# Performance work log

Measured on AMD Instinct MI355X. Metric: run time of the kernel, lower is better.

## Reference

```python
import jax, jax.numpy as jnp
import numpy as np

B = 256          # graph pairs
MAX = 64         # max_node_set_size
D = 128          # node_state_dim
E_DIM = 64       # edge embedding dim
NODE_F = 32
EDGE_F = 16
AVG_DEG = 8
PROP_STEPS = 3
TEMP = 0.1


def _sizes():
    qs = 32 + (np.arange(B) % 33)   # query graph sizes in [32,64]
    cs = 33 + (np.arange(B) % 32)   # corpus graph sizes in [33,64]
    return qs, cs


def setup_inputs() -> dict:
    key = jax.random.key(0)
    ks = jax.random.split(key, 12)
    qs, cs = _sizes()
    sizes = np.empty(2 * B, dtype=np.int64)
    sizes[0::2] = qs
    sizes[1::2] = cs
    offsets = np.concatenate([[0], np.cumsum(sizes)])
    N = int(offsets[-1])
    rng = np.random.RandomState(0)
    frm, to, pos = [], [], []
    for g in range(2 * B):
        o, s = int(offsets[g]), int(sizes[g])
        ne = AVG_DEG * s
        frm.append(rng.randint(0, s, ne) + o)
        to.append(rng.randint(0, s, ne) + o)
        b, isq = g // 2, (g % 2 == 0)
        base = (0 if isq else B * MAX) + b * MAX
        pos.append(base + np.arange(s))
    from_idx = jnp.asarray(np.concatenate(frm), dtype=jnp.int32)
    to_idx = jnp.asarray(np.concatenate(to), dtype=jnp.int32)
    node_to_pos = jnp.asarray(np.concatenate(pos), dtype=jnp.int32)
    Etot = int(from_idx.shape[0])

    def w(k, shape):
        return jax.random.normal(k, shape, jnp.float32) * (1.0 / np.sqrt(shape[0]))

    return {
        "node_features": jax.random.normal(ks[0], (N, NODE_F), jnp.float32),
        "edge_features": jax.random.normal(ks[1], (Etot, EDGE_F), jnp.float32),
        "from_idx": from_idx,
        "to_idx": to_idx,
        "node_to_pos": node_to_pos,
        "query_sizes": jnp.asarray(qs, jnp.int32),
        "corpus_sizes": jnp.asarray(cs, jnp.int32),
        "W_node": w(ks[2], (NODE_F, D)), "b_node": jnp.zeros((D,), jnp.float32),
        "W_edge": w(ks[3], (EDGE_F, E_DIM)), "b_edge": jnp.zeros((E_DIM,), jnp.float32),
        "W_msg1": w(ks[4], (2 * D + E_DIM, 2 * D)), "b_msg1": jnp.zeros((2 * D,), jnp.float32),
        "W_msg2": w(ks[5], (2 * D, 2 * D)), "b_msg2": jnp.zeros((2 * D,), jnp.float32),
        "W_upd": w(ks[6], (3 * D, D)), "b_upd": jnp.zeros((D,), jnp.float32),
        "Wa1": w(ks[7], (D, D)), "ba1": jnp.zeros((D,), jnp.float32),
        "Wa2": w(ks[8], (D, D)), "ba2": jnp.zeros((D,), jnp.float32),
    }


def reference(node_features, edge_features, from_idx, to_idx, node_to_pos,
              query_sizes, corpus_sizes, W_node, b_node, W_edge, b_edge,
              W_msg1, b_msg1, W_msg2, b_msg2, W_upd, b_upd, Wa1, ba1, Wa2, ba2):
    N = node_features.shape[0]
    # GraphEncoder: single-layer node / edge MLPs
    h = node_features @ W_node + b_node
    e = edge_features @ W_edge + b_edge
    # GraphPropLayer applied propagation_steps times (residual node update)
    for _ in range(PROP_STEPS):
        edge_in = jnp.concatenate([h[from_idx], h[to_idx], e], axis=-1)  # [E, 2D+E_DIM]
        msg = jax.nn.relu(edge_in @ W_msg1 + b_msg1) @ W_msg2 + b_msg2   # [E, 2D]
        agg = jax.ops.segment_sum(msg, to_idx, num_segments=N)           # [N, 2D]
        h = h + (jnp.concatenate([h, agg], axis=-1) @ W_upd + b_upd)
    # split_and_stack: scatter flat node states into padded [B, MAX, D] query/corpus stacks
    flat = jnp.zeros((2 * B * MAX, D), h.dtype).at[node_to_pos].set(h)
    stacked = flat.reshape(2, B, MAX, D)
    sq, sc = stacked[0], stacked[1]

    def att_feat(x):
        return jax.nn.relu(x @ Wa1 + ba1) @ Wa2 + ba2

    mq = (jnp.arange(MAX)[None, :] < query_sizes[:, None]).astype(h.dtype)   # [B,MAX]
    mc = (jnp.arange(MAX)[None, :] < corpus_sizes[:, None]).astype(h.dtype)
    tq = att_feat(sq) * mq[:, :, None]   # graph_size_to_mask_map masking
    tc = att_feat(sc) * mc[:, :, None]
    logits = jnp.einsum('bqd,bcd->bqc', tq, tc) / TEMP
    pair_mask = mq[:, :, None] * mc[:, None, :]
    logits = jnp.where(pair_mask > 0, logits, -1e9)
    q_to_c = jax.nn.softmax(logits, axis=-1) * mq[:, :, None]   # row-stochastic over corpus
    c_to_q = jax.nn.softmax(logits, axis=-2) * mc[:, None, :]   # column-stochastic over query
    # feature_alignment_score / reversed_feature_alignment_score (hinge alignment)
    q_score = -jax.nn.relu(sq - jnp.einsum('bqc,bcd->bqd', q_to_c, sc)).sum((1, 2))
    c_score = -jax.nn.relu(sc - jnp.einsum('bqc,bqd->bcd', c_to_q, sq)).sum((1, 2))
    return jnp.minimum(q_score, c_score)   # attention_mode = 'min'
```

## Files before the change

### kernel.cpp

```cpp
#include <hip/hip_runtime.h>

#define D 128
#define EDIM 64
#define NODE_F 32
#define EDGE_F 16
#define B_PAIRS 256
#define MAXN 64
#define PROP_STEPS 3

typedef __attribute__((ext_vector_type(4))) short short4v;
typedef __attribute__((ext_vector_type(8))) short short8;
typedef __attribute__((ext_vector_type(16))) float floatx16;

__device__ __forceinline__ short f2bf(float x) {
  unsigned u = __float_as_uint(x);
  u = (u + 0x7fff + ((u >> 16) & 1)) >> 16;
  return (short)u;
}

__device__ __forceinline__ float bf2f(short s) {
  return __uint_as_float(((unsigned)(unsigned short)s) << 16);
}

__global__ __launch_bounds__(256) void init_kernel(
    const float* __restrict__ W_node, const float* __restrict__ W_edge,
    const float* __restrict__ W1, const float* __restrict__ W2,
    const float* __restrict__ Wu,
    const float* __restrict__ Wa1, const float* __restrict__ Wa2,
    short* __restrict__ Wfn, short* __restrict__ Wfe,
    short* __restrict__ Wf1a, short* __restrict__ Wf1b, short* __restrict__ Wf1e,
    short* __restrict__ Wf2, short* __restrict__ Wfu,
    short* __restrict__ Wfa1, short* __restrict__ Wfa2,
    const int* __restrict__ to_idx, int* __restrict__ deg,
    int* __restrict__ inv, int E)
{
  int bid = blockIdx.x;
  int t = threadIdx.x;
  if (bid >= 916) {
    int b2 = bid - 916;
    for (int e = b2 * 256 + t; e < E; e += 256 * 256)
      atomicAdd(&deg[to_idx[e]], 1);
    for (int i = b2 * 256 + t; i < 2 * B_PAIRS * MAXN; i += 256 * 256)
      inv[i] = -1;
    return;
  }
  int idx = bid * 256 + t;
  if (idx < 4096) {
    int step = idx >> 11, hi = (idx >> 10) & 1;
    int n = (idx >> 3) & 127, j = idx & 7;
    int k = step * 16 + hi * 8 + j;
    Wfn[idx] = f2bf(W_node[(size_t)k * 128 + n]);
  } else if (idx < 5120) {
    int i = idx - 4096;
    int hi = (i >> 9) & 1, n = (i >> 3) & 63, j = i & 7;
    int k = hi * 8 + j;
    Wfe[i] = f2bf(W_edge[(size_t)k * 64 + n]);
  } else if (idx < 37888) {
    int i = idx - 5120;
    int step = i >> 12, hi = (i >> 11) & 1;
    int n = (i >> 3) & 255, j = i & 7;
    int k = step * 16 + hi * 8 + j;
    Wf1a[i] = f2bf(W1[(size_t)k * 256 + n]);
  } else if (idx < 70656) {
    int i = idx - 37888;
    int step = i >> 12, hi = (i >> 11) & 1;
    int n = (i >> 3) & 255, j = i & 7;
    int k = step * 16 + hi * 8 + j;
    Wf1b[i] = f2bf(W1[(size_t)(128 + k) * 256 + n]);
  } else if (idx < 87040) {
    int i = idx - 70656;
    int step = i >> 12, hi = (i >> 11) & 1;
    int n = (i >> 3) & 255, j = i & 7;
    int k = step * 16 + hi * 8 + j;
    Wf1e[i] = f2bf(W1[(size_t)(256 + k) * 256 + n]);
  } else if (idx < 152576) {
    int i = idx - 87040;
    int step = i >> 12, hi = (i >> 11) & 1;
    int n = (i >> 3) & 255, j = i & 7;
    int k = step * 16 + hi * 8 + j;
    Wf2[i] = f2bf(W2[(size_t)k * 256 + n]);
  } else if (idx < 201728) {
    int i = idx - 152576;
    int step = i >> 11, hi = (i >> 10) & 1;
    int n = (i >> 3) & 127, j = i & 7;
    int k = step * 16 + hi * 8 + j;
    Wfu[i] = f2bf(Wu[(size_t)k * 128 + n]);
  } else if (idx < 218112) {
    int i = idx - 201728;
    int step = i >> 11, hi = (i >> 10) & 1;
    int n = (i >> 3) & 127, j = i & 7;
    int k = step * 16 + hi * 8 + j;
    Wfa1[i] = f2bf(Wa1[(size_t)k * 128 + n]);
  } else if (idx < 234496) {
    int i = idx - 218112;
    int step = i >> 11, hi = (i >> 10) & 1;
    int n = (i >> 3) & 127, j = i & 7;
    int k = step * 16 + hi * 8 + j;
    Wfa2[i] = f2bf(Wa2[(size_t)k * 128 + n]);
  }
}

__global__ __launch_bounds__(1024) void scan1(const int* __restrict__ deg,
                                              int* __restrict__ partials, int N)
{
  __shared__ int red[16];
  int t = threadIdx.x;
  int n = blockIdx.x * 1024 + t;
  int v = (n < N) ? deg[n] : 0;
  for (int off = 32; off > 0; off >>= 1) v += __shfl_down(v, off);
  if ((t & 63) == 0) red[t >> 6] = v;
  __syncthreads();
  if (t == 0) {
    int s = 0;
    #pragma unroll
    for (int i = 0; i < 16; i++) s += red[i];
    partials[blockIdx.x] = s;
  }
}

__global__ __launch_bounds__(64) void scan2(int* __restrict__ partials,
                                            int* __restrict__ offsets, int B, int N)
{
  __shared__ int sp[64];
  int t = threadIdx.x;
  sp[t] = (t < B) ? partials[t] : 0;
  __syncthreads();
  if (t == 0) {
    int run = 0;
    for (int i = 0; i < B; i++) { int v = sp[i]; sp[i] = run; run += v; }
    offsets[N] = run;
  }
  __syncthreads();
  if (t < B) partials[t] = sp[t];
}

__global__ __launch_bounds__(1024) void scan3(const int* __restrict__ deg,
                                              const int* __restrict__ partials,
                                              int* __restrict__ offsets,
                                              int* __restrict__ cursor,
                                              int* __restrict__ zflag,
                                              const int* __restrict__ pos,
                                              int* __restrict__ inv, int N)
{
  __shared__ int s[1024];
  int t = threadIdx.x;
  int n = blockIdx.x * 1024 + t;
  int d = (n < N) ? deg[n] : 0;
  s[t] = d;
  __syncthreads();
  for (int off = 1; off < 1024; off <<= 1) {
    int v = 0;
    if (t >= off) v = s[t - off];
    __syncthreads();
    if (t >= off) s[t] += v;
    __syncthreads();
  }
  if (n < N) {
    int off = partials[blockIdx.x] + s[t] - d;
    offsets[n] = off; cursor[n] = off;
    zflag[n] = (d == 0) || ((off >> 6) != ((off + d - 1) >> 6)) ? 1 : 0;
    inv[pos[n]] = n;
  }
}

__global__ __launch_bounds__(256) void scatter_csr(const int* __restrict__ to_idx,
                                                   int* __restrict__ cursor,
                                                   int* __restrict__ elist, int E)
{
  for (int e = blockIdx.x * 256 + threadIdx.x; e < E; e += gridDim.x * 256) {
    int pos = atomicAdd(&cursor[to_idx[e]], 1);
    elist[pos] = e;
  }
}

__global__ __launch_bounds__(256, 3) void enc_nodes_p(
    const float* __restrict__ nf, const short* __restrict__ Wfn,
    const float* __restrict__ b_node, float* __restrict__ h,
    short* __restrict__ hb,
    const short* __restrict__ Wf1a, const short* __restrict__ Wf1b,
    short* __restrict__ P1f, short* __restrict__ P2f, int N)
{
  __shared__ short sN[32 * 40];
  __shared__ short sH[32 * 136];
  int t = threadIdx.x;
  int ln = t & 63, w = t >> 6;
  int l31 = ln & 31, hi = ln >> 5;
  int n0 = blockIdx.x * 32;

  {
    int r = t >> 3, q = t & 7;
    float4 v = {0.f, 0.f, 0.f, 0.f};
    if (n0 + r < N) v = *(const float4*)(nf + (size_t)(n0 + r) * 32 + q * 4);
    short4v s;
    s[0] = f2bf(v.x); s[1] = f2bf(v.y); s[2] = f2bf(v.z); s[3] = f2bf(v.w);
    *(short4v*)(sN + r * 40 + q * 4) = s;
  }
  __syncthreads();

  int col = w * 32 + l31;
  {
    floatx16 acc;
    #pragma unroll
    for (int i = 0; i < 16; i++) acc[i] = 0.f;
    #pragma unroll
    for (int step = 0; step < 2; step++) {
      short8 a = *(const short8*)(sN + l31 * 40 + step * 16 + hi * 8);
      short8 b = *(const short8*)(Wfn + (size_t)(step * 2 + hi) * 1024 + col * 8);
      acc = __builtin_amdgcn_mfma_f32_32x32x16_bf16(a, b, acc, 0, 0, 0);
    }
    float bv = b_node[col];
    #pragma unroll
    for (int reg = 0; reg < 16; reg++) {
      int row = (reg & 3) + 8 * (reg >> 2) + 4 * hi;
      int n = n0 + row;
      float v = acc[reg] + bv;
      short bf = f2bf(v);
      if (n < N) {
        h[(size_t)n * 128 + col] = v;
        hb[(size_t)n * 128 + col] = bf;
      }
      sH[row * 136 + col] = bf;
    }
  }
  __syncthreads();

  int cb = w * 64;
  const int arow = l31 * 136;
  const int bc0 = (cb + l31) * 8, bc1 = (cb + 32 + l31) * 8;
  floatx16 acc[2][2];
  #pragma unroll
  for (int o = 0; o < 2; o++)
    #pragma unroll
    for (int ct = 0; ct < 2; ct++)
      #pragma unroll
      for (int i = 0; i < 16; i++) acc[o][ct][i] = 0.f;

  #pragma unroll
  for (int step = 0; step < 8; step++) {
    short8 a = *(const short8*)(sH + arow + step * 16 + hi * 8);
    short8 ba0 = *(const short8*)(Wf1a + (size_t)(step * 2 + hi) * 2048 + bc0);
    short8 ba1 = *(const short8*)(Wf1a + (size_t)(step * 2 + hi) * 2048 + bc1);
    short8 bb0 = *(const short8*)(Wf1b + (size_t)(step * 2 + hi) * 2048 + bc0);
    short8 bb1 = *(const short8*)(Wf1b + (size_t)(step * 2 + hi) * 2048 + bc1);
    acc[0][0] = __builtin_amdgcn_mfma_f32_32x32x16_bf16(a, ba0, acc[0][0], 0, 0, 0);
    acc[0][1] = __builtin_amdgcn_mfma_f32_32x32x16_bf16(a, ba1, acc[0][1], 0, 0, 0);
    acc[1][0] = __builtin_amdgcn_mfma_f32_32x32x16_bf16(a, bb0, acc[1][0], 0, 0, 0);
    acc[1][1] = __builtin_amdgcn_mfma_f32_32x32x16_bf16(a, bb1, acc[1][1], 0, 0, 0);
  }

  #pragma unroll
  for (int ct = 0; ct < 2; ct++) {
    int pcol = cb + ct * 32 + l31;
    #pragma unroll
    for (int reg = 0; reg < 16; reg++) {
      int row = (reg & 3) + 8 * (reg >> 2) + 4 * hi;
      int n = n0 + row;
      if (n < N) {
        P1f[(size_t)n * 256 + pcol] = f2bf(acc[0][ct][reg]);
        P2f[(size_t)n * 256 + pcol] = f2bf(acc[1][ct][reg]);
      }
    }
  }
}

__global__ __launch_bounds__(256, 4) void pe_fused(
    const float* __restrict__ ef, const int* __restrict__ elist,
    const short* __restrict__ Wfe, const float* __restrict__ b_edge,
    const short* __restrict__ Wf1e, const float* __restrict__ b1,
    short* __restrict__ Pe, int E)
{
  __shared__ short sE[64 * 24];
  __shared__ short sF[64 * 72];
  __shared__ int eid_s[64];

  int t = threadIdx.x;
  int ln = t & 63, w = t >> 6;
  int l31 = ln & 31, hi = ln >> 5;
  int e0 = blockIdx.x * 64;

  if (t < 64) eid_s[t] = (e0 + t < E) ? elist[e0 + t] : 0;
  __syncthreads();

  {
    int r = t >> 2, q = t & 3;
    float4 v = *(const float4*)(ef + (size_t)eid_s[r] * 16 + q * 4);
    short4v s;
    s[0] = f2bf(v.x); s[1] = f2bf(v.y); s[2] = f2bf(v.z); s[3] = f2bf(v.w);
    *(short4v*)(sE + r * 24 + q * 4) = s;
  }
  __syncthreads();

  {
    int rowb = (w & 1) * 32, cbq = (w >> 1) * 32;
    floatx16 acc;
    #pragma unroll
    for (int i = 0; i < 16; i++) acc[i] = 0.f;
    short8 a = *(const short8*)(sE + (rowb + l31) * 24 + hi * 8);
    short8 b = *(const short8*)(Wfe + (size_t)hi * 512 + (cbq + l31) * 8);
    acc = __builtin_amdgcn_mfma_f32_32x32x16_bf16(a, b, acc, 0, 0, 0);
    int col = cbq + l31;
    float bv = b_edge[col];
    #pragma unroll
    for (int reg = 0; reg < 16; reg++) {
      int row = rowb + (reg & 3) + 8 * (reg >> 2) + 4 * hi;
      sF[row * 72 + col] = f2bf(acc[reg] + bv);
    }
  }
  __syncthreads();

  const int cb = w * 64;
  const int bc0 = (cb + l31) * 8, bc1 = (cb + 32 + l31) * 8;
  floatx16 acc[2][2];
  #pragma unroll
  for (int rg = 0; rg < 2; rg++)
    #pragma unroll
    for (int ct = 0; ct < 2; ct++)
      #pragma unroll
      for (int i = 0; i < 16; i++) acc[rg][ct][i] = 0.f;

  #pragma unroll
  for (int step = 0; step < 4; step++) {
    short8 a0 = *(const short8*)(sF + l31 * 72 + step * 16 + hi * 8);
    short8 a1 = *(const short8*)(sF + (32 + l31) * 72 + step * 16 + hi * 8);
    short8 b0 = *(const short8*)(Wf1e + (size_t)(step * 2 + hi) * 2048 + bc0);
    short8 b1v = *(const short8*)(Wf1e + (size_t)(step * 2 + hi) * 2048 + bc1);
    acc[0][0] = __builtin_amdgcn_mfma_f32_32x32x16_bf16(a0, b0,  acc[0][0], 0, 0, 0);
    acc[0][1] = __builtin_amdgcn_mfma_f32_32x32x16_bf16(a0, b1v, acc[0][1], 0, 0, 0);
    acc[1][0] = __builtin_amdgcn_mfma_f32_32x32x16_bf16(a1, b0,  acc[1][0], 0, 0, 0);
    acc[1][1] = __builtin_amdgcn_mfma_f32_32x32x16_bf16(a1, b1v, acc[1][1], 0, 0, 0);
  }

  #pragma unroll
  for (int rg = 0; rg < 2; rg++)
    #pragma unroll
    for (int ct = 0; ct < 2; ct++) {
      int col = cb + ct * 32 + l31;
      float bv = b1[col];
      #pragma unroll
      for (int reg = 0; reg < 16; reg++) {
        int row = rg * 32 + (reg & 3) + 8 * (reg >> 2) + 4 * hi;
        Pe[(size_t)(e0 + row) * 256 + col] = f2bf(acc[rg][ct][reg] + bv);
      }
    }
}

__global__ __launch_bounds__(256, 4) void msg_agg(
    const short* __restrict__ P1f, const short* __restrict__ P2f,
    const short* __restrict__ Pe,
    const int* __restrict__ from_idx, const int* __restrict__ to_idx,
    const int* __restrict__ elist, const int* __restrict__ offsets,
    float* __restrict__ agg, int E)
{
  __shared__ short sA[64 * 264];
  __shared__ int from_s[64], to_s[64];
  __shared__ int rend_s[64], inter_s[64];

  int t = threadIdx.x;
  int e0 = blockIdx.x * 64;

  if (t < 64) {
    int idx = e0 + t;
    int eid = (idx < E) ? elist[idx] : 0;
    from_s[t] = from_idx[eid];
    to_s[t] = (idx < E) ? to_idx[eid] : -1;
  }
  __syncthreads();

  if (t < 64) {
    int nd = to_s[t];
    bool head = (t == 0) || (nd != to_s[t - 1]);
    if (head && nd >= 0) {
      int re = t + 1;
      while (re < 64 && to_s[re] == nd) re++;
      rend_s[t] = re;
      inter_s[t] = (offsets[nd] == e0 + t) && (offsets[nd + 1] == e0 + re) ? 1 : 0;
    }
  }

  for (int i = t; i < 2048; i += 256) {
    int r = i >> 5, c8 = (i & 31) * 8;
    int nd = to_s[r]; if (nd < 0) nd = 0;
    short8 a = *(const short8*)(P1f + (size_t)from_s[r] * 256 + c8);
    short8 b = *(const short8*)(P2f + (size_t)nd * 256 + c8);
    short8 c = *(const short8*)(Pe + (size_t)(e0 + r) * 256 + c8);
    short8 o;
    #pragma unroll
    for (int j = 0; j < 8; j++)
      o[j] = f2bf(fmaxf(bf2f(a[j]) + bf2f(b[j]) + bf2f(c[j]), 0.f));
    *(short8*)(sA + r * 264 + c8) = o;
  }
  __syncthreads();

  {
    int c = t;
    for (int r = 0; r < 64; ) {
      int nd = to_s[r];
      if (nd < 0) break;
      int re = rend_s[r];
      float a = 0.f;
      for (int i = r; i < re; i++)
        a += bf2f(sA[i * 264 + c]);
      float* dst = agg + (size_t)nd * 256 + c;
      if (inter_s[r]) *dst = a;
      else unsafeAtomicAdd(dst, a);
      r = re;
    }
  }
}

__global__ __launch_bounds__(256, 3) void update_mfma_p(
    float* __restrict__ h, short* __restrict__ hbf, float* __restrict__ agg,
    const short* __restrict__ Wf2, const float* __restrict__ b2,
    const int* __restrict__ deg,
    const short* __restrict__ Wfu, const float* __restrict__ bu,
    const short* __restrict__ Wf1a, const short* __restrict__ Wf1b,
    short* __restrict__ P1f, short* __restrict__ P2f,
    const int* __restrict__ zflag, int want_p, int N)
{
  __shared__ short sA[32 * 392];
  __shared__ short sS[32 * 264];
  __shared__ int zf_s[32];
  __shared__ int deg_s[32];

  int t = threadIdx.x;
  int ln = t & 63, w = t >> 6;
  int l31 = ln & 31, hi = ln >> 5;
  int n0 = blockIdx.x * 32;

  if (t < 32) {
    zf_s[t] = (n0 + t < N) ? zflag[n0 + t] : 0;
    deg_s[t] = (n0 + t < N) ? deg[n0 + t] : 0;
  }

  for (int i = t; i < 512; i += 256) {
    int r = i >> 4, c = i & 15;
    short8 v = {0, 0, 0, 0, 0, 0, 0, 0};
    if (n0 + r < N) v = *(const short8*)(hbf + (size_t)(n0 + r) * 128 + c * 8);
    *(short8*)(sA + r * 392 + c * 8) = v;
  }
  for (int i = t; i < 2048; i += 256) {
    int r = i >> 6, c4 = i & 63;
    int2 pk = {0, 0};
    if (n0 + r < N) {
      float4 v = *(const float4*)(agg + (size_t)(n0 + r) * 256 + c4 * 4);
      pk.x = (int)(unsigned short)f2bf(v.x) | ((int)(unsigned short)f2bf(v.y) << 16);
      pk.y = (int)(unsigned short)f2bf(v.z) | ((int)(unsigned short)f2bf(v.w) << 16);
    }
    *(int2*)(sS + r * 264 + c4 * 4) = pk;
  }
  __syncthreads();

  {
    float4 z = {0.f, 0.f, 0.f, 0.f};
    for (int i = t; i < 2048; i += 256) {
      int r = i >> 6, c4 = i & 63;
      if (n0 + r < N && zf_s[r])
        *(float4*)(agg + (size_t)(n0 + r) * 256 + c4 * 4) = z;
    }
  }

  {
    int cb2 = w * 64;
    const int bc0 = (cb2 + l31) * 8, bc1 = (cb2 + 32 + l31) * 8;
    floatx16 macc[2];
    #pragma unroll
    for (int ct = 0; ct < 2; ct++)
      #pragma unroll
      for (int i = 0; i < 16; i++) macc[ct][i] = 0.f;

    #pragma unroll
    for (int step = 0; step < 16; step++) {
      short8 a = *(const short8*)(sS + l31 * 264 + step * 16 + hi * 8);
      short8 b0 = *(const short8*)(Wf2 + (size_t)(step * 2 + hi) * 2048 + bc0);
      short8 b1v = *(const short8*)(Wf2 + (size_t)(step * 2 + hi) * 2048 + bc1);
      macc[0] = __builtin_amdgcn_mfma_f32_32x32x16_bf16(a, b0,  macc[0], 0, 0, 0);
      macc[1] = __builtin_amdgcn_mfma_f32_32x32x16_bf16(a, b1v, macc[1], 0, 0, 0);
    }

    #pragma unroll
    for (int ct = 0; ct < 2; ct++) {
      int col = cb2 + ct * 32 + l31;
      float bv2 = b2[col];
      #pragma unroll
      for (int reg = 0; reg < 16; reg++) {
        int row = (reg & 3) + 8 * (reg >> 2) + 4 * hi;
        sA[row * 392 + 128 + col] = f2bf(macc[ct][reg] + (float)deg_s[row] * bv2);
      }
    }
  }
  __syncthreads();

  const int arow = l31 * 392;
  const int bcol = (w * 32 + l31) * 8;

  floatx16 acc;
  #pragma unroll
  for (int i = 0; i < 16; i++) acc[i] = 0.f;

  {
    short8 bbuf[3];
    #pragma unroll
    for (int s = 0; s < 3; s++)
      bbuf[s] = *(const short8*)(Wfu + (size_t)(s * 2 + hi) * 1024 + bcol);
    short8 abuf[2];
    abuf[0] = *(const short8*)(sA + arow + hi * 8);
    #pragma unroll
    for (int step = 0; step < 24; step++) {
      if (step + 1 < 24)
        abuf[(step + 1) & 1] = *(const short8*)(sA + arow + (step + 1) * 16 + hi * 8);
      acc = __builtin_amdgcn_mfma_f32_32x32x16_bf16(abuf[step & 1], bbuf[step % 3], acc, 0, 0, 0);
      if (step + 3 < 24)
        bbuf[step % 3] = *(const short8*)(Wfu + (size_t)((step + 3) * 2 + hi) * 1024 + bcol);
    }
  }

  __syncthreads();

  int col = w * 32 + l31;
  float bv = bu[col];
  #pragma unroll
  for (int reg = 0; reg < 16; reg++) {
    int row = (reg & 3) + 8 * (reg >> 2) + 4 * hi;
    int n = n0 + row;
    float nv = 0.f;
    if (n < N) nv = h[(size_t)n * 128 + col] + acc[reg] + bv;
    short bf = f2bf(nv);
    if (n < N) {
      h[(size_t)n * 128 + col] = nv;
      hbf[(size_t)n * 128 + col] = bf;
    }
    sA[row * 392 + col] = bf;
  }

  if (!want_p) return;
  __syncthreads();

  int cb = w * 64;
  const int bc0 = (cb + l31) * 8, bc1 = (cb + 32 + l31) * 8;
  floatx16 pacc[2][2];
  #pragma unroll
  for (int o = 0; o < 2; o++)
    #pragma unroll
    for (int ct = 0; ct < 2; ct++)
      #pragma unroll
      for (int i = 0; i < 16; i++) pacc[o][ct][i] = 0.f;

  #pragma unroll
  for (int step = 0; step < 8; step++) {
    short8 a = *(const short8*)(sA + arow + step * 16 + hi * 8);
    short8 ba0 = *(const short8*)(Wf1a + (size_t)(step * 2 + hi) * 2048 + bc0);
    short8 ba1 = *(const short8*)(Wf1a + (size_t)(step * 2 + hi) * 2048 + bc1);
    short8 bb0 = *(const short8*)(Wf1b + (size_t)(step * 2 + hi) * 2048 + bc0);
    short8 bb1 = *(const short8*)(Wf1b + (size_t)(step * 2 + hi) * 2048 + bc1);
    pacc[0][0] = __builtin_amdgcn_mfma_f32_32x32x16_bf16(a, ba0, pacc[0][0], 0, 0, 0);
    pacc[0][1] = __builtin_amdgcn_mfma_f32_32x32x16_bf16(a, ba1, pacc[0][1], 0, 0, 0);
    pacc[1][0] = __builtin_amdgcn_mfma_f32_32x32x16_bf16(a, bb0, pacc[1][0], 0, 0, 0);
    pacc[1][1] = __builtin_amdgcn_mfma_f32_32x32x16_bf16(a, bb1, pacc[1][1], 0, 0, 0);
  }

  #pragma unroll
  for (int ct = 0; ct < 2; ct++) {
    int pcol = cb + ct * 32 + l31;
    #pragma unroll
    for (int reg = 0; reg < 16; reg++) {
      int row = (reg & 3) + 8 * (reg >> 2) + 4 * hi;
      int n = n0 + row;
      if (n < N) {
        P1f[(size_t)n * 256 + pcol] = f2bf(pacc[0][ct][reg]);
        P2f[(size_t)n * 256 + pcol] = f2bf(pacc[1][ct][reg]);
      }
    }
  }
}

__global__ __launch_bounds__(256, 3) void stack_attfeat(
    const float* __restrict__ h, const int* __restrict__ inv,
    const short* __restrict__ Wfa1, const float* __restrict__ ba1,
    const short* __restrict__ Wfa2, const float* __restrict__ ba2,
    const int* __restrict__ qsizes, const int* __restrict__ csizes,
    float* __restrict__ flat, short* __restrict__ flatT, short* __restrict__ tfb)
{
  __shared__ short sA[64 * 136];
  __shared__ int nd_s[64];

  int t = threadIdx.x;
  int ln = t & 63, w = t >> 6;
  int l31 = ln & 31, hi = ln >> 5;
  int r0 = blockIdx.x * 64;

  if (t < 64) nd_s[t] = inv[r0 + t];
  __syncthreads();

  for (int i = t; i < 1024; i += 256) {
    int r = i >> 4, c = (i & 15) * 8;
    int nd = nd_s[r];
    float4 v0 = {0.f, 0.f, 0.f, 0.f}, v1 = {0.f, 0.f, 0.f, 0.f};
    if (nd >= 0) {
      v0 = *(const float4*)(h + (size_t)nd * 128 + c);
      v1 = *(const float4*)(h + (size_t)nd * 128 + c + 4);
    }
    *(float4*)(flat + (size_t)(r0 + r) * 128 + c) = v0;
    *(float4*)(flat + (size_t)(r0 + r) * 128 + c + 4) = v1;
    short8 s;
    s[0] = f2bf(v0.x); s[1] = f2bf(v0.y); s[2] = f2bf(v0.z); s[3] = f2bf(v0.w);
    s[4] = f2bf(v1.x); s[5] = f2bf(v1.y); s[6] = f2bf(v1.z); s[7] = f2bf(v1.w);
    *(short8*)(sA + r * 136 + c) = s;
  }
  __syncthreads();

  for (int i = t; i < 8192; i += 256) {
    int d = i >> 6, r = i & 63;
    flatT[(size_t)blockIdx.x * 8192 + d * 64 + r] = sA[r * 136 + d];
  }

  const int arow0 = l31 * 136, arow1 = (32 + l31) * 136;
  const int bcol = (w * 32 + l31) * 8;
  int col = w * 32 + l31;

  floatx16 acc[2];
  #pragma unroll
  for (int rg = 0; rg < 2; rg++)
    #pragma unroll
    for (int i = 0; i < 16; i++) acc[rg][i] = 0.f;

  #pragma unroll
  for (int step = 0; step < 8; step++) {
    short8 a0 = *(const short8*)(sA + arow0 + step * 16 + hi * 8);
    short8 a1 = *(const short8*)(sA + arow1 + step * 16 + hi * 8);
    short8 bfr = *(const short8*)(Wfa1 + (size_t)(step * 2 + hi) * 1024 + bcol);
    acc[0] = __builtin_amdgcn_mfma_f32_32x32x16_bf16(a0, bfr, acc[0], 0, 0, 0);
    acc[1] = __builtin_amdgcn_mfma_f32_32x32x16_bf16(a1, bfr, acc[1], 0, 0, 0);
  }

  __syncthreads();
  {
    float bv = ba1[col];
    #pragma unroll
    for (int rg = 0; rg < 2; rg++)
      #pragma unroll
      for (int reg = 0; reg < 16; reg++) {
        int row = rg * 32 + (reg & 3) + 8 * (reg >> 2) + 4 * hi;
        sA[row * 136 + col] = f2bf(fmaxf(acc[rg][reg] + bv, 0.f));
      }
  }
  __syncthreads();

  floatx16 acc2[2];
  #pragma unroll
  for (int rg = 0; rg < 2; rg++)
    #pragma unroll
    for (int i = 0; i < 16; i++) acc2[rg][i] = 0.f;

  #pragma unroll
  for (int step = 0; step < 8; step++) {
    short8 a0 = *(const short8*)(sA + arow0 + step * 16 + hi * 8);
    short8 a1 = *(const short8*)(sA + arow1 + step * 16 + hi * 8);
    short8 bfr = *(const short8*)(Wfa2 + (size_t)(step * 2 + hi) * 1024 + bcol);
    acc2[0] = __builtin_amdgcn_mfma_f32_32x32x16_bf16(a0, bfr, acc2[0], 0, 0, 0);
    acc2[1] = __builtin_amdgcn_mfma_f32_32x32x16_bf16(a1, bfr, acc2[1], 0, 0, 0);
  }

  {
    float bv = ba2[col];
    #pragma unroll
    for (int rg = 0; rg < 2; rg++)
      #pragma unroll
      for (int reg = 0; reg < 16; reg++) {
        int row = r0 + rg * 32 + (reg & 3) + 8 * (reg >> 2) + 4 * hi;
        int part = row >> 14, b = (row >> 6) & 255, pp = row & 63;
        int sz = part ? csizes[b] : qsizes[b];
        float m = (pp < sz) ? 1.f : 0.f;
        tfb[(size_t)row * 128 + col] = f2bf((acc2[rg][reg] + bv) * m);
      }
  }
}

__global__ __launch_bounds__(256, 3) void score_kernel(
    const short* __restrict__ tfb, const float* __restrict__ flat,
    const short* __restrict__ flatT,
    const int* __restrict__ qsizes, const int* __restrict__ csizes,
    float* __restrict__ out)
{
  __shared__ float SL[64 * 65];
  __shared__ float SP2[64 * 65];
  __shared__ float red[8];

  int b = blockIdx.x, t = threadIdx.x;
  int ln = t & 63, w = t >> 6;
  int l31 = ln & 31, hi = ln >> 5;
  const short* tqb = tfb + (size_t)b * 8192;
  const short* tcb = tfb + (size_t)(256 + b) * 8192;
  const float* sq = flat + (size_t)b * 8192;
  const float* sc = flat + (size_t)(256 + b) * 8192;
  const short* sqT = flatT + (size_t)b * 8192;
  const short* scT = flatT + (size_t)(256 + b) * 8192;
  int qs = qsizes[b], cs = csizes[b];

  {
    int rowb = (w & 1) * 32, cbq = (w >> 1) * 32;
    floatx16 acc;
    #pragma unroll
    for (int i = 0; i < 16; i++) acc[i] = 0.f;
    #pragma unroll
    for (int step = 0; step < 8; step++) {
      short8 a  = *(const short8*)(tqb + (size_t)(rowb + l31) * 128 + step * 16 + hi * 8);
      short8 bf = *(const short8*)(tcb + (size_t)(cbq + l31) * 128 + step * 16 + hi * 8);
      acc = __builtin_amdgcn_mfma_f32_32x32x16_bf16(a, bf, acc, 0, 0, 0);
    }
    int ccol = cbq + l31;
    #pragma unroll
    for (int reg = 0; reg < 16; reg++) {
      int qrow = rowb + (reg & 3) + 8 * (reg >> 2) + 4 * hi;
      SL[qrow * 65 + ccol] = (qrow < qs && ccol < cs) ? acc[reg] * 10.0f : -1e9f;
    }
  }
  __syncthreads();

  float rmax = -1e30f, rsum = 0.f;
  if (t < 64) {
    int q = t;
    if (q < qs) {
      for (int c = 0; c < 64; c++) rmax = fmaxf(rmax, SL[q * 65 + c]);
      for (int c = 0; c < 64; c++) rsum += __expf(SL[q * 65 + c] - rmax);
    }
  } else if (t < 128) {
    int c = t - 64;
    if (c < cs) {
      float m = -1e30f;
      for (int q = 0; q < 64; q++) m = fmaxf(m, SL[q * 65 + c]);
      float s = 0.f;
      for (int q = 0; q < 64; q++) s += __expf(SL[q * 65 + c] - m);
      float inv = 1.0f / s;
      for (int q = 0; q < 64; q++) SP2[q * 65 + c] = __expf(SL[q * 65 + c] - m) * inv;
    } else {
      for (int q = 0; q < 64; q++) SP2[q * 65 + c] = 0.f;
    }
  }
  __syncthreads();

  if (t < 64) {
    int q = t;
    if (q < qs) {
      float inv = 1.0f / rsum;
      for (int c = 0; c < 64; c++) SL[q * 65 + c] = __expf(SL[q * 65 + c] - rmax) * inv;
    } else {
      for (int c = 0; c < 64; c++) SL[q * 65 + c] = 0.f;
    }
  }
  __syncthreads();

  int dcol = w * 32 + l31;
  floatx16 accq[2], accc[2];
  #pragma unroll
  for (int rt = 0; rt < 2; rt++) {
    #pragma unroll
    for (int i = 0; i < 16; i++) { accq[rt][i] = 0.f; accc[rt][i] = 0.f; }
  }

  #pragma unroll
  for (int rt = 0; rt < 2; rt++) {
    #pragma unroll
    for (int step = 0; step < 4; step++) {
      int kb = step * 16 + hi * 8;
      int row = rt * 32 + l31;
      short8 a;
      #pragma unroll
      for (int j = 0; j < 8; j++) a[j] = f2bf(SL[row * 65 + kb + j]);
      short8 bf = *(const short8*)(scT + (size_t)dcol * 64 + kb);
      accq[rt] = __builtin_amdgcn_mfma_f32_32x32x16_bf16(a, bf, accq[rt], 0, 0, 0);
    }
  }
  #pragma unroll
  for (int rt = 0; rt < 2; rt++) {
    #pragma unroll
    for (int step = 0; step < 4; step++) {
      int kb = step * 16 + hi * 8;
      int crow = rt * 32 + l31;
      short8 a;
      #pragma unroll
      for (int j = 0; j < 8; j++) a[j] = f2bf(SP2[(kb + j) * 65 + crow]);
      short8 bf = *(const short8*)(sqT + (size_t)dcol * 64 + kb);
      accc[rt] = __builtin_amdgcn_mfma_f32_32x32x16_bf16(a, bf, accc[rt], 0, 0, 0);
    }
  }

  float qpart = 0.f, cpart = 0.f;
  #pragma unroll
  for (int rt = 0; rt < 2; rt++) {
    #pragma unroll
    for (int reg = 0; reg < 16; reg++) {
      int row = rt * 32 + (reg & 3) + 8 * (reg >> 2) + 4 * hi;
      qpart += fmaxf(sq[(size_t)row * 128 + dcol] - accq[rt][reg], 0.f);
      cpart += fmaxf(sc[(size_t)row * 128 + dcol] - accc[rt][reg], 0.f);
    }
  }

  for (int off = 32; off > 0; off >>= 1) {
    qpart += __shfl_down(qpart, off);
    cpart += __shfl_down(cpart, off);
  }
  if ((t & 63) == 0) { red[w] = qpart; red[w + 4] = cpart; }
  __syncthreads();
  if (t == 0) {
    float qsum = red[0] + red[1] + red[2] + red[3];
    float csum = red[4] + red[5] + red[6] + red[7];
    out[b] = fminf(-qsum, -csum);
  }
}

extern "C" void kernel_launch(void* const* d_in, const int* in_sizes, int n_in,
                              void* d_out, int out_size, void* d_ws, size_t ws_size,
                              hipStream_t stream)
{
  const float* nf  = (const float*)d_in[0];
  const float* ef  = (const float*)d_in[1];
  const int* from_idx = (const int*)d_in[2];
  const int* to_idx   = (const int*)d_in[3];
  const int* pos      = (const int*)d_in[4];
  const int* qsz      = (const int*)d_in[5];
  const int* csz      = (const int*)d_in[6];
  const float* W_node = (const float*)d_in[7];
  const float* b_node = (const float*)d_in[8];
  const float* W_edge = (const float*)d_in[9];
  const float* b_edge = (const float*)d_in[10];
  const float* W1 = (const float*)d_in[11];
  const float* b1 = (const float*)d_in[12];
  const float* W2 = (const float*)d_in[13];
  const float* b2 = (const float*)d_in[14];
  const float* Wu = (const float*)d_in[15];
  const float* bu = (const float*)d_in[16];
  const float* Wa1 = (const float*)d_in[17];
  const float* ba1 = (const float*)d_in[18];
  const float* Wa2 = (const float*)d_in[19];
  const float* ba2 = (const float*)d_in[20];
  float* out = (float*)d_out;

  int N = in_sizes[0] / NODE_F;
  int E = in_sizes[1] / EDGE_F;
  int Epad = (E + 63) & ~63;
  int PAD = 2 * B_PAIRS * MAXN;
  int NB = (N + 1023) / 1024;

  float* h    = (float*)d_ws;
  float* agg  = h + (size_t)N * D;
  short* hb   = (short*)(agg + (size_t)N * 256);
  short* P1f  = hb + (size_t)N * D;
  short* P2f  = P1f + (size_t)N * 256;
  short* Wfn  = P2f + (size_t)N * 256;
  short* Wfe  = Wfn + 4096;
  short* Wf1a = Wfe + 1024;
  short* Wf1b = Wf1a + 32768;
  short* Wf1e = Wf1b + 32768;
  short* Wf2  = Wf1e + 16384;
  short* Wfu  = Wf2 + 65536;
  short* Wfa1 = Wfu + 49152;
  short* Wfa2 = Wfa1 + 16384;
  int*   deg     = (int*)(Wfa2 + 16384);
  int*   offsets = deg + N;
  int*   cursor  = offsets + N + 1;
  int*   elist   = cursor + N;
  int*   inv     = elist + E;
  int*   zflag   = inv + PAD;
  int*   partials = zflag + N;
  uintptr_t pb = ((uintptr_t)(partials + 64) + 15) & ~(uintptr_t)15;
  short* Pe = (short*)pb;
  float* flat  = (float*)Pe;
  short* flatT = (short*)(flat + (size_t)PAD * D);
  short* tfb16 = flatT + (size_t)PAD * D;

  hipMemsetAsync(deg, 0, (size_t)N * sizeof(int), stream);
  init_kernel<<<916 + 256, 256, 0, stream>>>(
      W_node, W_edge, W1, W2, Wu, Wa1, Wa2,
      Wfn, Wfe, Wf1a, Wf1b, Wf1e, Wf2, Wfu, Wfa1, Wfa2,
      to_idx, deg, inv, E);
  scan1<<<NB, 1024, 0, stream>>>(deg, partials, N);
  scan2<<<1, 64, 0, stream>>>(partials, offsets, NB, N);
  scan3<<<NB, 1024, 0, stream>>>(deg, partials, offsets, cursor, zflag, pos, inv, N);
  scatter_csr<<<256, 256, 0, stream>>>(to_idx, cursor, elist, E);

  enc_nodes_p<<<(N + 31) / 32, 256, 0, stream>>>(nf, Wfn, b_node, h, hb,
                                                 Wf1a, Wf1b, P1f, P2f, N);
  pe_fused<<<Epad / 64, 256, 0, stream>>>(ef, elist, Wfe, b_edge, Wf1e, b1, Pe, E);

  hipMemsetAsync(agg, 0, (size_t)N * 256 * sizeof(float), stream);

  for (int s = 0; s < PROP_STEPS; s++) {
    msg_agg<<<Epad / 64, 256, 0, stream>>>(P1f, P2f, Pe, from_idx, to_idx, elist, offsets,
                                           agg, E);
    update_mfma_p<<<(N + 31) / 32, 256, 0, stream>>>(h, hb, agg, Wf2, b2, deg,
                                                     Wfu, bu, Wf1a, Wf1b, P1f, P2f, zflag,
                                                     (s + 1 < PROP_STEPS) ? 1 : 0, N);
  }

  stack_attfeat<<<PAD / 64, 256, 0, stream>>>(h, inv, Wfa1, ba1, Wfa2, ba2,
                                              qsz, csz, flat, flatT, tfb16);
  score_kernel<<<B_PAIRS, 256, 0, stream>>>(tfb16, flat, flatT, qsz, csz, out);
}
```

Measured before the change: 456.0 us.

## Fuse message aggregation into node update kernel with shared-memory CSR accumulation

Merges the per-edge message aggregation kernel into the node update kernel. Each block of 32 nodes walks its own CSR edge range and accumulates messages in shared memory instead of doing global atomics into an fp32 agg buffer. This removes the agg round-trip, the zero-flag logic, the memset and one launch per step. P1 is now double-buffered, reusing the agg region, because other blocks still read the previous P1 while this block writes the new one. In exchange the grid is node-based, so blocks with many edges serialize in 32-edge chunks and shared memory per block grows, which may cut occupancy.

```diff
diff --git a/kernel.cpp b/kernel.cpp
--- a/kernel.cpp
+++ b/kernel.cpp
@@ -138,7 +138,6 @@
                                               const int* __restrict__ partials,
                                               int* __restrict__ offsets,
                                               int* __restrict__ cursor,
-                                              int* __restrict__ zflag,
                                               const int* __restrict__ pos,
                                               int* __restrict__ inv, int N)
 {
@@ -158,7 +157,6 @@
   if (n < N) {
     int off = partials[blockIdx.x] + s[t] - d;
     offsets[n] = off; cursor[n] = off;
-    zflag[n] = (d == 0) || ((off >> 6) != ((off + d - 1) >> 6)) ? 1 : 0;
     inv[pos[n]] = n;
   }
 }
@@ -344,119 +342,93 @@
     }
 }
 
-__global__ __launch_bounds__(256, 4) void msg_agg(
-    const short* __restrict__ P1f, const short* __restrict__ P2f,
-    const short* __restrict__ Pe,
+__global__ __launch_bounds__(256, 3) void msg_upd(
+    float* __restrict__ h, short* __restrict__ hbf,
+    const short* __restrict__ P1in, short* __restrict__ P1out,
+    short* __restrict__ P2f, const short* __restrict__ Pe,
     const int* __restrict__ from_idx, const int* __restrict__ to_idx,
     const int* __restrict__ elist, const int* __restrict__ offsets,
-    float* __restrict__ agg, int E)
-{
-  __shared__ short sA[64 * 264];
-  __shared__ int from_s[64], to_s[64];
-  __shared__ int rend_s[64], inter_s[64];
-
-  int t = threadIdx.x;
-  int e0 = blockIdx.x * 64;
-
-  if (t < 64) {
-    int idx = e0 + t;
-    int eid = (idx < E) ? elist[idx] : 0;
-    from_s[t] = from_idx[eid];
-    to_s[t] = (idx < E) ? to_idx[eid] : -1;
-  }
-  __syncthreads();
-
-  if (t < 64) {
-    int nd = to_s[t];
-    bool head = (t == 0) || (nd != to_s[t - 1]);
-    if (head && nd >= 0) {
-      int re = t + 1;
-      while (re < 64 && to_s[re] == nd) re++;
-      rend_s[t] = re;
-      inter_s[t] = (offsets[nd] == e0 + t) && (offsets[nd + 1] == e0 + re) ? 1 : 0;
-    }
-  }
-
-  for (int i = t; i < 2048; i += 256) {
-    int r = i >> 5, c8 = (i & 31) * 8;
-    int nd = to_s[r]; if (nd < 0) nd = 0;
-    short8 a = *(const short8*)(P1f + (size_t)from_s[r] * 256 + c8);
-    short8 b = *(const short8*)(P2f + (size_t)nd * 256 + c8);
-    short8 c = *(const short8*)(Pe + (size_t)(e0 + r) * 256 + c8);
-    short8 o;
-    #pragma unroll
-    for (int j = 0; j < 8; j++)
-      o[j] = f2bf(fmaxf(bf2f(a[j]) + bf2f(b[j]) + bf2f(c[j]), 0.f));
-    *(short8*)(sA + r * 264 + c8) = o;
-  }
-  __syncthreads();
-
-  {
-    int c = t;
-    for (int r = 0; r < 64; ) {
-      int nd = to_s[r];
-      if (nd < 0) break;
-      int re = rend_s[r];
-      float a = 0.f;
-      for (int i = r; i < re; i++)
-        a += bf2f(sA[i * 264 + c]);
-      float* dst = agg + (size_t)nd * 256 + c;
-      if (inter_s[r]) *dst = a;
-      else unsafeAtomicAdd(dst, a);
-      r = re;
-    }
-  }
-}
-
-__global__ __launch_bounds__(256, 3) void update_mfma_p(
-    float* __restrict__ h, short* __restrict__ hbf, float* __restrict__ agg,
+    const int* __restrict__ deg,
     const short* __restrict__ Wf2, const float* __restrict__ b2,
-    const int* __restrict__ deg,
     const short* __restrict__ Wfu, const float* __restrict__ bu,
     const short* __restrict__ Wf1a, const short* __restrict__ Wf1b,
-    short* __restrict__ P1f, short* __restrict__ P2f,
-    const int* __restrict__ zflag, int want_p, int N)
-{
-  __shared__ short sA[32 * 392];
-  __shared__ short sS[32 * 264];
-  __shared__ int zf_s[32];
-  __shared__ int deg_s[32];
+    int want_p, int N)
+{
+  __shared__ float aggL[32 * 256];
+  __shared__ short sStage[32 * 264];
+  __shared__ int to_s[32], from_s[32], deg_s[32];
 
   int t = threadIdx.x;
   int ln = t & 63, w = t >> 6;
   int l31 = ln & 31, hi = ln >> 5;
   int n0 = blockIdx.x * 32;
-
-  if (t < 32) {
-    zf_s[t] = (n0 + t < N) ? zflag[n0 + t] : 0;
-    deg_s[t] = (n0 + t < N) ? deg[n0 + t] : 0;
-  }
+  int nend = (n0 + 32 < N) ? n0 + 32 : N;
+
+  if (t < 32) deg_s[t] = (n0 + t < N) ? deg[n0 + t] : 0;
+  for (int i = t; i < 8192; i += 256) aggL[i] = 0.f;
+  int e_begin = offsets[n0];
+  int e_end = offsets[nend];
+  __syncthreads();
+
+  for (int e0 = e_begin; e0 < e_end; e0 += 32) {
+    if (t < 32) {
+      int idx = e0 + t;
+      if (idx < e_end) {
+        int eid = elist[idx];
+        from_s[t] = from_idx[eid];
+        to_s[t] = to_idx[eid] - n0;
+      } else {
+        to_s[t] = -1;
+      }
+    }
+    __syncthreads();
+
+    for (int i = t; i < 1024; i += 256) {
+      int r = i >> 5, c8 = (i & 31) * 8;
+      int nd = to_s[r];
+      if (nd >= 0) {
+        short8 a = *(const short8*)(P1in + (size_t)from_s[r] * 256 + c8);
+        short8 b = *(const short8*)(P2f + (size_t)(n0 + nd) * 256 + c8);
+        short8 c = *(const short8*)(Pe + (size_t)(e0 + r) * 256 + c8);
+        short8 o;
+        #pragma unroll
+        for (int j = 0; j < 8; j++)
+          o[j] = f2bf(fmaxf(bf2f(a[j]) + bf2f(b[j]) + bf2f(c[j]), 0.f));
+        *(short8*)(sStage + r * 264 + c8) = o;
+      }
+    }
+    __syncthreads();
+
+    {
+      int c = t;
+      for (int r = 0; r < 32; ) {
+        int nd = to_s[r];
+        if (nd < 0) break;
+        int re = r + 1;
+        while (re < 32 && to_s[re] == nd) re++;
+        float a = 0.f;
+        for (int i2 = r; i2 < re; i2++)
+          a += bf2f(sStage[i2 * 264 + c]);
+        aggL[nd * 256 + c] += a;
+        r = re;
+      }
+    }
+    __syncthreads();
+  }
+
+  short* sS = sStage;
+  #pragma unroll
+  for (int k = 0; k < 32; k++)
+    sS[k * 264 + t] = f2bf(aggL[k * 256 + t]);
+  __syncthreads();
+
+  short* sA = (short*)aggL;
 
   for (int i = t; i < 512; i += 256) {
     int r = i >> 4, c = i & 15;
     short8 v = {0, 0, 0, 0, 0, 0, 0, 0};
     if (n0 + r < N) v = *(const short8*)(hbf + (size_t)(n0 + r) * 128 + c * 8);
     *(short8*)(sA + r * 392 + c * 8) = v;
-  }
-  for (int i = t; i < 2048; i += 256) {
-    int r = i >> 6, c4 = i & 63;
-    int2 pk = {0, 0};
-    if (n0 + r < N) {
-      float4 v = *(const float4*)(agg + (size_t)(n0 + r) * 256 + c4 * 4);
-      pk.x = (int)(unsigned short)f2bf(v.x) | ((int)(unsigned short)f2bf(v.y) << 16);
-      pk.y = (int)(unsigned short)f2bf(v.z) | ((int)(unsigned short)f2bf(v.w) << 16);
-    }
-    *(int2*)(sS + r * 264 + c4 * 4) = pk;
-  }
-  __syncthreads();
-
-  {
-    float4 z = {0.f, 0.f, 0.f, 0.f};
-    for (int i = t; i < 2048; i += 256) {
-      int r = i >> 6, c4 = i & 63;
-      if (n0 + r < N && zf_s[r])
-        *(float4*)(agg + (size_t)(n0 + r) * 256 + c4 * 4) = z;
-    }
   }
 
   {
@@ -566,7 +538,7 @@
       int row = (reg & 3) + 8 * (reg >> 2) + 4 * hi;
       int n = n0 + row;
       if (n < N) {
-        P1f[(size_t)n * 256 + pcol] = f2bf(pacc[0][ct][reg]);
+        P1out[(size_t)n * 256 + pcol] = f2bf(pacc[0][ct][reg]);
         P2f[(size_t)n * 256 + pcol] = f2bf(pacc[1][ct][reg]);
       }
     }
@@ -842,8 +814,8 @@
   int NB = (N + 1023) / 1024;
 
   float* h    = (float*)d_ws;
-  float* agg  = h + (size_t)N * D;
-  short* hb   = (short*)(agg + (size_t)N * 256);
+  float* aggv = h + (size_t)N * D;
+  short* hb   = (short*)(aggv + (size_t)N * 256);
   short* P1f  = hb + (size_t)N * D;
   short* P2f  = P1f + (size_t)N * 256;
   short* Wfn  = P2f + (size_t)N * 256;
@@ -868,6 +840,9 @@
   short* flatT = (short*)(flat + (size_t)PAD * D);
   short* tfb16 = flatT + (size_t)PAD * D;
 
+  short* P1a = P1f;
+  short* P1b = (short*)aggv;
+
   hipMemsetAsync(deg, 0, (size_t)N * sizeof(int), stream);
   init_kernel<<<916 + 256, 256, 0, stream>>>(
       W_node, W_edge, W1, W2, Wu, Wa1, Wa2,
@@ -875,21 +850,20 @@
       to_idx, deg, inv, E);
   scan1<<<NB, 1024, 0, stream>>>(deg, partials, N);
   scan2<<<1, 64, 0, stream>>>(partials, offsets, NB, N);
-  scan3<<<NB, 1024, 0, stream>>>(deg, partials, offsets, cursor, zflag, pos, inv, N);
+  scan3<<<NB, 1024, 0, stream>>>(deg, partials, offsets, cursor, pos, inv, N);
   scatter_csr<<<256, 256, 0, stream>>>(to_idx, cursor, elist, E);
 
   enc_nodes_p<<<(N + 31) / 32, 256, 0, stream>>>(nf, Wfn, b_node, h, hb,
-                                                 Wf1a, Wf1b, P1f, P2f, N);
+                                                 Wf1a, Wf1b, P1a, P2f, N);
   pe_fused<<<Epad / 64, 256, 0, stream>>>(ef, elist, Wfe, b_edge, Wf1e, b1, Pe, E);
 
-  hipMemsetAsync(agg, 0, (size_t)N * 256 * sizeof(float), stream);
-
   for (int s = 0; s < PROP_STEPS; s++) {
-    msg_agg<<<Epad / 64, 256, 0, stream>>>(P1f, P2f, Pe, from_idx, to_idx, elist, offsets,
-                                           agg, E);
-    update_mfma_p<<<(N + 31) / 32, 256, 0, stream>>>(h, hb, agg, Wf2, b2, deg,
-                                                     Wfu, bu, Wf1a, Wf1b, P1f, P2f, zflag,
-                                                     (s + 1 < PROP_STEPS) ? 1 : 0, N);
+    const short* pin = (s & 1) ? P1b : P1a;
+    short* pout = (s & 1) ? P1a : P1b;
+    msg_upd<<<(N + 31) / 32, 256, 0, stream>>>(h, hb, pin, pout, P2f, Pe,
+                                               from_idx, to_idx, elist, offsets, deg,
+                                               Wf2, b2, Wfu, bu, Wf1a, Wf1b,
+                                               (s + 1 < PROP_STEPS) ? 1 : 0, N);
   }
 
   stack_attfeat<<<PAD / 64, 256, 0, stream>>>(h, inv, Wfa1, ba1, Wfa2, ba2,
```

Result: slower. 589.5 us (+29.3%).

## Reduce edge messages in registers per warp, merge runs in LDS slots

Applied to the files above, without the earlier changes.

The message-aggregation kernel no longer writes the 64x256 bf16 relu-sum tile to shared memory and re-reads it column-wise. Each warp now walks 8 consecutive edges, prefetching the next edge's vectors while it accumulates same-destination runs in fp32 registers. A run that covers a node's whole edge range is stored directly to global memory. Other runs are merged through small shared-memory slots with LDS atomics and then written out or globally atomically added. The change cuts LDS traffic and the bf16 rounding of intermediate messages, and raises the occupancy hint, at the cost of more branching and shared atomics.

```diff
diff --git a/kernel.cpp b/kernel.cpp
--- a/kernel.cpp
+++ b/kernel.cpp
@@ -344,66 +344,101 @@
     }
 }
 
-__global__ __launch_bounds__(256, 4) void msg_agg(
+__global__ __launch_bounds__(256, 6) void msg_agg(
     const short* __restrict__ P1f, const short* __restrict__ P2f,
     const short* __restrict__ Pe,
     const int* __restrict__ from_idx, const int* __restrict__ to_idx,
     const int* __restrict__ elist, const int* __restrict__ offsets,
     float* __restrict__ agg, int E)
 {
-  __shared__ short sA[64 * 264];
   __shared__ int from_s[64], to_s[64];
-  __shared__ int rend_s[64], inter_s[64];
+  __shared__ float aggS[9 * 256];
+  __shared__ int slotnd[9];
 
   int t = threadIdx.x;
-  int e0 = blockIdx.x * 64;
+  int gb = blockIdx.x * 64;
 
   if (t < 64) {
-    int idx = e0 + t;
+    int idx = gb + t;
     int eid = (idx < E) ? elist[idx] : 0;
     from_s[t] = from_idx[eid];
     to_s[t] = (idx < E) ? to_idx[eid] : -1;
   }
-  __syncthreads();
-
-  if (t < 64) {
-    int nd = to_s[t];
-    bool head = (t == 0) || (nd != to_s[t - 1]);
-    if (head && nd >= 0) {
-      int re = t + 1;
-      while (re < 64 && to_s[re] == nd) re++;
-      rend_s[t] = re;
-      inter_s[t] = (offsets[nd] == e0 + t) && (offsets[nd + 1] == e0 + re) ? 1 : 0;
-    }
-  }
-
-  for (int i = t; i < 2048; i += 256) {
-    int r = i >> 5, c8 = (i & 31) * 8;
-    int nd = to_s[r]; if (nd < 0) nd = 0;
-    short8 a = *(const short8*)(P1f + (size_t)from_s[r] * 256 + c8);
-    short8 b = *(const short8*)(P2f + (size_t)nd * 256 + c8);
-    short8 c = *(const short8*)(Pe + (size_t)(e0 + r) * 256 + c8);
-    short8 o;
-    #pragma unroll
-    for (int j = 0; j < 8; j++)
-      o[j] = f2bf(fmaxf(bf2f(a[j]) + bf2f(b[j]) + bf2f(c[j]), 0.f));
-    *(short8*)(sA + r * 264 + c8) = o;
-  }
-  __syncthreads();
-
-  {
-    int c = t;
-    for (int r = 0; r < 64; ) {
-      int nd = to_s[r];
-      if (nd < 0) break;
-      int re = rend_s[r];
-      float a = 0.f;
-      for (int i = r; i < re; i++)
-        a += bf2f(sA[i * 264 + c]);
-      float* dst = agg + (size_t)nd * 256 + c;
-      if (inter_s[r]) *dst = a;
-      else unsafeAtomicAdd(dst, a);
-      r = re;
+  if (t < 9) slotnd[t] = -1;
+  for (int i = t; i < 2304; i += 256) aggS[i] = 0.f;
+  __syncthreads();
+
+  const int w0 = (t >> 5) * 8;
+  const int c8 = (t & 31) * 8;
+
+  float acc[8];
+  #pragma unroll
+  for (int k = 0; k < 8; k++) acc[k] = 0.f;
+  int cur = -1, ra = w0;
+
+  auto flushrun = [&](int nd, int rra, int rrb) {
+    if (nd < 0 || rrb <= rra) return;
+    int ss = offsets[nd], se = offsets[nd + 1];
+    if (ss == gb + rra && se == gb + rrb) {
+      float* dst = agg + (size_t)nd * 256 + c8;
+      #pragma unroll
+      for (int k = 0; k < 8; k++) dst[k] = acc[k];
+    } else {
+      int ra0 = ss - gb;
+      int slot = (ra0 < 0) ? 0 : ((ra0 >> 3) + 1);
+      slotnd[slot] = nd;
+      #pragma unroll
+      for (int k = 0; k < 8; k++)
+        atomicAdd(&aggS[slot * 256 + c8 + k], acc[k]);
+    }
+  };
+
+  int nd_next = to_s[w0];
+  short8 na = {0,0,0,0,0,0,0,0}, nb = na, nc = na;
+  if (nd_next >= 0) {
+    na = *(const short8*)(P1f + (size_t)from_s[w0] * 256 + c8);
+    nb = *(const short8*)(P2f + (size_t)nd_next * 256 + c8);
+    nc = *(const short8*)(Pe + (size_t)(gb + w0) * 256 + c8);
+  }
+  #pragma unroll
+  for (int j = 0; j < 8; j++) {
+    int r = w0 + j;
+    int nd = nd_next;
+    short8 a = na, b = nb, c = nc;
+    if (j < 7) {
+      nd_next = to_s[r + 1];
+      if (nd_next >= 0) {
+        na = *(const short8*)(P1f + (size_t)from_s[r + 1] * 256 + c8);
+        nb = *(const short8*)(P2f + (size_t)nd_next * 256 + c8);
+        nc = *(const short8*)(Pe + (size_t)(gb + r + 1) * 256 + c8);
+      }
+    }
+    if (nd != cur) {
+      flushrun(cur, ra, r);
+      cur = nd; ra = r;
+      #pragma unroll
+      for (int k = 0; k < 8; k++) acc[k] = 0.f;
+    }
+    if (nd >= 0) {
+      #pragma unroll
+      for (int k = 0; k < 8; k++)
+        acc[k] += fmaxf(bf2f(a[k]) + bf2f(b[k]) + bf2f(c[k]), 0.f);
+    }
+  }
+  flushrun(cur, ra, w0 + 8);
+  __syncthreads();
+
+  {
+    int col = t;
+    #pragma unroll
+    for (int s = 0; s < 9; s++) {
+      int nd = slotnd[s];
+      if (nd < 0) continue;
+      int ss = offsets[nd], se = offsets[nd + 1];
+      float v = aggS[s * 256 + col];
+      float* dst = agg + (size_t)nd * 256 + col;
+      if (ss >= gb && se <= gb + 64) *dst = v;
+      else unsafeAtomicAdd(dst, v);
     }
   }
 }
```

After: 520.9 us. +14.2%, slower.
